# Kernel tuning notes

Hardware: AMD Instinct MI355X
Metric: run time of the kernel (lower is better)

Reference implementation:

```python
import jax, jax.numpy as jnp
import numpy as np

B, S, E = 2, 2048, 2048
H, D = 16, 128  # num_heads, head_dim = E // H


def setup_inputs() -> dict:
    key = jax.random.key(0)
    ks = jax.random.split(key, 5)
    hidden_states = jax.random.normal(ks[0], (B, S, E), dtype=jnp.float32) * 0.02
    wq = jax.random.normal(ks[1], (E, E), dtype=jnp.float32) * 0.02
    wk = jax.random.normal(ks[2], (E, E), dtype=jnp.float32) * 0.02
    wv = jax.random.normal(ks[3], (E, E), dtype=jnp.float32) * 0.02
    wo = jax.random.normal(ks[4], (E, E), dtype=jnp.float32) * 0.02
    bo = jnp.zeros((E,), dtype=jnp.float32)
    return {"hidden_states": hidden_states, "wq": wq, "wk": wk, "wv": wv, "wo": wo, "bo": bo}


def _split_heads(x):
    # [B, S, E] -> [B, H, S, D]
    return x.reshape(B, S, H, D).transpose(0, 2, 1, 3)


def reference(hidden_states, wq, wk, wv, wo, bo):
    q = _split_heads(hidden_states @ wq)  # [B,H,S,D]
    k = _split_heads(hidden_states @ wk)
    v = _split_heads(hidden_states @ wv)

    # GPT-Neo: no 1/sqrt(d) scaling; scores computed in fp32
    attn_weights = jnp.einsum("bhqd,bhkd->bhqk", q.astype(jnp.float32), k.astype(jnp.float32))

    causal_mask = jnp.tril(jnp.ones((S, S), dtype=bool))  # bias[:, :, :S, :S]
    # Faithful quirk: masked positions get the GLOBAL MIN of attn_weights, not -inf
    mask_value = jnp.min(attn_weights)
    attn_weights = jnp.where(causal_mask, attn_weights, mask_value)

    attn_weights = jax.nn.softmax(attn_weights, axis=-1).astype(v.dtype)
    attn_output = jnp.einsum("bhqk,bhkd->bhqd", attn_weights, v)  # [B,H,S,D]

    # merge heads: [B,H,S,D] -> [B,S,E]
    attn_output = attn_output.transpose(0, 2, 1, 3).reshape(B, S, E)
    attn_output = attn_output @ wo + bo
    return attn_output
```

## Files before the change

### kernel.cpp

```cpp
#include <hip/hip_runtime.h>

typedef unsigned short u16;
typedef unsigned int   u32;
typedef __attribute__((ext_vector_type(4))) float f32x4;
typedef __attribute__((ext_vector_type(4))) u32   u32x4;
typedef __attribute__((ext_vector_type(8))) __bf16 bf16x8;

#define S_LEN 2048
#define EMB   2048
#define NH    16
#define HD    128
#define NBH   32
#define MTOT  4096
#define NBMIN 512

__device__ __forceinline__ u16 f2bf(float f) {
    u32 u = __float_as_uint(f);
    return (u16)((u + 0x7FFFu + ((u >> 16) & 1u)) >> 16);
}
__device__ __forceinline__ float bf2f(u16 v) {
    return __uint_as_float(((u32)v) << 16);
}
__device__ __forceinline__ bf16x8 ld_frag(const u16* p) {
    return __builtin_bit_cast(bf16x8, *(const u32x4*)p);
}
__device__ __forceinline__ void gld_lds16(const void* g, void* l) {
    __builtin_amdgcn_global_load_lds(
        (__attribute__((address_space(1))) void*)(g),
        (__attribute__((address_space(3))) void*)(l), 16, 0, 0);
}

__global__ __launch_bounds__(256) void cast_x_kernel(
    const float* __restrict__ X, u16* __restrict__ Xb)
{
    const size_t i = ((size_t)blockIdx.x * 256 + threadIdx.x) * 8;
    float4 a = *(const float4*)&X[i];
    float4 b = *(const float4*)&X[i + 4];
    u32x4 o;
    o.x = (u32)f2bf(a.x) | ((u32)f2bf(a.y) << 16);
    o.y = (u32)f2bf(a.z) | ((u32)f2bf(a.w) << 16);
    o.z = (u32)f2bf(b.x) | ((u32)f2bf(b.y) << 16);
    o.w = (u32)f2bf(b.z) | ((u32)f2bf(b.w) << 16);
    *(u32x4*)&Xb[i] = o;
}

__global__ __launch_bounds__(256) void transpose_cast_w_kernel(
    const float* __restrict__ W0, const float* __restrict__ W1,
    const float* __restrict__ W2, const float* __restrict__ W3,
    u16* __restrict__ T0, u16* __restrict__ T1,
    u16* __restrict__ T2, u16* __restrict__ T3)
{
    __shared__ float Ls[64][68];
    const int t = threadIdx.x;
    const int n0 = blockIdx.x * 64, k0 = blockIdx.y * 64;
    const int z = blockIdx.z;
    const float* __restrict__ W = (z == 0) ? W0 : (z == 1) ? W1 : (z == 2) ? W2 : W3;
    u16* __restrict__ T = (z == 0) ? T0 : (z == 1) ? T1 : (z == 2) ? T2 : T3;

#pragma unroll
    for (int p = 0; p < 4; ++p) {
        const int r = (t >> 4) + 16 * p;
        const int c = (t & 15) * 4;
        *(float4*)&Ls[r][c] = *(const float4*)&W[(size_t)(k0 + r) * EMB + n0 + c];
    }
    __syncthreads();
    const int nl = t >> 2, q = t & 3;
    u32 pk[8];
#pragma unroll
    for (int j = 0; j < 8; ++j) {
        u16 lo = f2bf(Ls[q * 16 + 2 * j][nl]);
        u16 hi = f2bf(Ls[q * 16 + 2 * j + 1][nl]);
        pk[j] = (u32)lo | ((u32)hi << 16);
    }
    u32x4 o0 = {pk[0], pk[1], pk[2], pk[3]};
    u32x4 o1 = {pk[4], pk[5], pk[6], pk[7]};
    u16* dst = &T[(size_t)(n0 + nl) * EMB + k0 + q * 16];
    *(u32x4*)&dst[0] = o0;
    *(u32x4*)&dst[8] = o1;
}

__global__ __launch_bounds__(256) void transpose_v_kernel(
    const u16* __restrict__ V, u16* __restrict__ Vt)
{
    __shared__ u16 Ls[64][72];
    const int t = threadIdx.x;
    const int s0 = blockIdx.x * 64, d0 = blockIdx.y * 64, bh = blockIdx.z;
    const u16* __restrict__ src0 = V + ((size_t)bh * S_LEN) * HD;
    {
        const int r = t >> 2, c0 = (t & 3) * 16;
        const u16* src = &src0[(size_t)(s0 + r) * HD + d0 + c0];
        *(u32x4*)&Ls[r][c0]     = *(const u32x4*)&src[0];
        *(u32x4*)&Ls[r][c0 + 8] = *(const u32x4*)&src[8];
    }
    __syncthreads();
    const int dl = t >> 2, q = t & 3;
    u32 pk[8];
#pragma unroll
    for (int j = 0; j < 8; ++j) {
        u16 lo = Ls[q * 16 + 2 * j][dl];
        u16 hi = Ls[q * 16 + 2 * j + 1][dl];
        pk[j] = (u32)lo | ((u32)hi << 16);
    }
    u32x4 o0 = {pk[0], pk[1], pk[2], pk[3]};
    u32x4 o1 = {pk[4], pk[5], pk[6], pk[7]};
    u16* dst = &Vt[((size_t)bh * HD + d0 + dl) * S_LEN + s0 + q * 16];
    *(u32x4*)&dst[0] = o0;
    *(u32x4*)&dst[8] = o1;
}

__global__ __launch_bounds__(256) void gemm_qkv_mfma(
    const u16* __restrict__ Xb,
    const u16* __restrict__ Wtq, const u16* __restrict__ Wtk,
    const u16* __restrict__ Wtv,
    u16* __restrict__ Qo, u16* __restrict__ Ko, u16* __restrict__ Vo)
{
    __shared__ __attribute__((aligned(16))) u16 As[128 * 64];
    __shared__ __attribute__((aligned(16))) u16 Bs[128 * 64];
    const int t = threadIdx.x;
    const int w = t >> 6, lane = t & 63;
    const int wy = w >> 1, wx = w & 1;
    const int n0 = blockIdx.x * 128, m0 = blockIdx.y * 128;
    const int z = blockIdx.z;
    const u16* __restrict__ Wt = (z == 0) ? Wtq : (z == 1) ? Wtk : Wtv;
    u16* __restrict__ O = (z == 0) ? Qo : (z == 1) ? Ko : Vo;

    const int srow8 = lane >> 3;
    const int scol  = ((lane & 7) ^ srow8) * 8;
    const int fm = lane & 15, fk = (lane >> 4) * 8;
    const int key = (fm & 7) * 8;

    const u16* Ag = &Xb[(size_t)(m0 + w * 32 + srow8) * EMB + scol];
    const u16* Bg = &Wt[(size_t)(n0 + w * 32 + srow8) * EMB + scol];
    u16* const Al = &As[(w * 32) * 64];
    u16* const Bl = &Bs[(w * 32) * 64];

    f32x4 acc[4][4];
#pragma unroll
    for (int i = 0; i < 4; ++i)
#pragma unroll
        for (int j = 0; j < 4; ++j) acc[i][j] = (f32x4)0.0f;

    for (int k0 = 0; k0 < EMB; k0 += 64) {
        __syncthreads();
        gld_lds16(Ag + k0,               Al);
        gld_lds16(Ag + k0 + 8 * EMB,     Al + 8 * 64);
        gld_lds16(Ag + k0 + 16 * EMB,    Al + 16 * 64);
        gld_lds16(Ag + k0 + 24 * EMB,    Al + 24 * 64);
        gld_lds16(Bg + k0,               Bl);
        gld_lds16(Bg + k0 + 8 * EMB,     Bl + 8 * 64);
        gld_lds16(Bg + k0 + 16 * EMB,    Bl + 16 * 64);
        gld_lds16(Bg + k0 + 24 * EMB,    Bl + 24 * 64);
        __syncthreads();
#pragma unroll
        for (int dk2 = 0; dk2 < 2; ++dk2) {
            bf16x8 af[4], bfr[4];
#pragma unroll
            for (int mi = 0; mi < 4; ++mi)
                af[mi] = ld_frag(&As[(64 * wy + 16 * mi + fm) * 64
                                     + ((dk2 * 32 + fk) ^ key)]);
#pragma unroll
            for (int ni = 0; ni < 4; ++ni)
                bfr[ni] = ld_frag(&Bs[(64 * wx + 16 * ni + fm) * 64
                                      + ((dk2 * 32 + fk) ^ key)]);
#pragma unroll
            for (int mi = 0; mi < 4; ++mi)
#pragma unroll
                for (int ni = 0; ni < 4; ++ni)
                    acc[mi][ni] = __builtin_amdgcn_mfma_f32_16x16x32_bf16(
                        af[mi], bfr[ni], acc[mi][ni], 0, 0, 0);
        }
    }

    const int q4 = (lane >> 4) * 4;
#pragma unroll
    for (int mi = 0; mi < 4; ++mi)
#pragma unroll
        for (int ni = 0; ni < 4; ++ni) {
            const int n = n0 + 64 * wx + 16 * ni + (lane & 15);
            const int h = n >> 7, d = n & 127;
#pragma unroll
            for (int r = 0; r < 4; ++r) {
                const int m = m0 + 64 * wy + 16 * mi + q4 + r;
                const int bb = m >> 11, s = m & 2047;
                O[(((size_t)(bb * NH + h) * S_LEN) + s) * HD + d] = f2bf(acc[mi][ni][r]);
            }
        }
}

__global__ __launch_bounds__(256) void gemm_out_mfma(
    const u16* __restrict__ Ab, const u16* __restrict__ Wto,
    const float* __restrict__ bias, float* __restrict__ Out)
{
    __shared__ __attribute__((aligned(16))) u16 As[128 * 64];
    __shared__ __attribute__((aligned(16))) u16 Bs[64 * 64];
    const int t = threadIdx.x;
    const int w = t >> 6, lane = t & 63;
    const int wy = w >> 1, wx = w & 1;
    const int n0 = blockIdx.x * 64, m0 = blockIdx.y * 128;

    const int srow8 = lane >> 3;
    const int scol  = ((lane & 7) ^ srow8) * 8;
    const int fm = lane & 15, fk = (lane >> 4) * 8;
    const int key = (fm & 7) * 8;

    const u16* Ag = &Ab[(size_t)(m0 + w * 32 + srow8) * EMB + scol];
    const u16* Bg = &Wto[(size_t)(n0 + w * 16 + srow8) * EMB + scol];
    u16* const Al = &As[(w * 32) * 64];
    u16* const Bl = &Bs[(w * 16) * 64];

    f32x4 acc[4][2];
#pragma unroll
    for (int i = 0; i < 4; ++i)
#pragma unroll
        for (int j = 0; j < 2; ++j) acc[i][j] = (f32x4)0.0f;

    for (int k0 = 0; k0 < EMB; k0 += 64) {
        __syncthreads();
        gld_lds16(Ag + k0,               Al);
        gld_lds16(Ag + k0 + 8 * EMB,     Al + 8 * 64);
        gld_lds16(Ag + k0 + 16 * EMB,    Al + 16 * 64);
        gld_lds16(Ag + k0 + 24 * EMB,    Al + 24 * 64);
        gld_lds16(Bg + k0,               Bl);
        gld_lds16(Bg + k0 + 8 * EMB,     Bl + 8 * 64);
        __syncthreads();
#pragma unroll
        for (int dk2 = 0; dk2 < 2; ++dk2) {
            bf16x8 af[4], bfr[2];
#pragma unroll
            for (int mi = 0; mi < 4; ++mi)
                af[mi] = ld_frag(&As[(64 * wy + 16 * mi + fm) * 64
                                     + ((dk2 * 32 + fk) ^ key)]);
#pragma unroll
            for (int ni = 0; ni < 2; ++ni)
                bfr[ni] = ld_frag(&Bs[(32 * wx + 16 * ni + fm) * 64
                                      + ((dk2 * 32 + fk) ^ key)]);
#pragma unroll
            for (int mi = 0; mi < 4; ++mi)
#pragma unroll
                for (int ni = 0; ni < 2; ++ni)
                    acc[mi][ni] = __builtin_amdgcn_mfma_f32_16x16x32_bf16(
                        af[mi], bfr[ni], acc[mi][ni], 0, 0, 0);
        }
    }

    const int q4 = (lane >> 4) * 4;
#pragma unroll
    for (int mi = 0; mi < 4; ++mi)
#pragma unroll
        for (int ni = 0; ni < 2; ++ni) {
            const int n = n0 + 32 * wx + 16 * ni + (lane & 15);
            const float bv = bias[n];
#pragma unroll
            for (int r = 0; r < 4; ++r) {
                const int m = m0 + 64 * wy + 16 * mi + q4 + r;
                Out[(size_t)m * EMB + n] = acc[mi][ni][r] + bv;
            }
        }
}

__global__ __launch_bounds__(128) void vchunk_sum_kernel(
    const u16* __restrict__ V, float* __restrict__ csum)
{
    const int chunk = blockIdx.x, bh = blockIdx.y, d = threadIdx.x;
    const u16* vb = V + ((size_t)bh * S_LEN + chunk * 64) * HD + d;
    float s = 0.0f;
    for (int r = 0; r < 64; ++r) s += bf2f(vb[(size_t)r * HD]);
    csum[((size_t)bh * 32 + chunk) * HD + d] = s;
}

__global__ __launch_bounds__(128) void vsuffix_kernel(
    const u16* __restrict__ V, const float* __restrict__ csum,
    u16* __restrict__ vsuf)
{
    const int chunk = blockIdx.x, bh = blockIdx.y, d = threadIdx.x;
    float run = 0.0f;
    for (int c = 31; c > chunk; --c)
        run += csum[((size_t)bh * 32 + c) * HD + d];
    const size_t base = ((size_t)bh * S_LEN + chunk * 64) * HD + d;
    for (int r = 63; r >= 0; --r) {
        vsuf[base + (size_t)r * HD] = f2bf(run);
        run += bf2f(V[base + (size_t)r * HD]);
    }
}

__global__ __launch_bounds__(256) void attn_mfma(
    const u16* __restrict__ Q, const u16* __restrict__ K,
    const u16* __restrict__ Vt,
    u16* __restrict__ pacc0, u16* __restrict__ pacc1,
    float* __restrict__ den_p, float* __restrict__ blockmin)
{
    __shared__ __attribute__((aligned(16))) u16 Ps[128 * 136];
    __shared__ __attribute__((aligned(16))) u16 Cs[2][128 * 64];
    __shared__ float den_l[2][128];
    __shared__ float smn[256];

    const int t = threadIdx.x;
    const int w = t >> 6, lane = t & 63;
    const int wy = w >> 1, wx = w & 1;

    const int d_id = blockIdx.y * 16 + blockIdx.x;
    const int f_log = (d_id & 7) * 64 + (d_id >> 3);
    const int pp = (f_log & 15) >> 1, hpar = f_log & 1;
    const int bh = f_log >> 4;
    const int b = bh >> 4, h = bh & 15;

    const u16* __restrict__ Kg  = K + (size_t)bh * S_LEN * HD;
    const u16* __restrict__ Vtg = Vt + (size_t)bh * HD * S_LEN;
    u16* __restrict__ pacc = hpar ? pacc1 : pacc0;

    const int srow8 = lane >> 3;
    const int scol  = ((lane & 7) ^ srow8) * 8;
    const int fm = lane & 15, fk = (lane >> 4) * 8;
    const int key = (fm & 7) * 8;
    const int q4 = (lane >> 4) * 4;

#define STAGE_K(b_, j0_, h_) do { \
        const u16* g_ = &Kg[(size_t)((j0_) + w * 32 + srow8) * HD + (h_) * 64 + scol]; \
        u16* l_ = &Cs[b_][(w * 32) * 64]; \
        gld_lds16(g_,           l_); \
        gld_lds16(g_ + 8 * HD,  l_ + 8 * 64); \
        gld_lds16(g_ + 16 * HD, l_ + 16 * 64); \
        gld_lds16(g_ + 24 * HD, l_ + 24 * 64); } while (0)
#define STAGE_V(b_, j0_, h_) do { \
        const u16* g_ = &Vtg[(size_t)(w * 32 + srow8) * S_LEN + (j0_) + (h_) * 64 + scol]; \
        u16* l_ = &Cs[b_][(w * 32) * 64]; \
        gld_lds16(g_,              l_); \
        gld_lds16(g_ + 8 * S_LEN,  l_ + 8 * 64); \
        gld_lds16(g_ + 16 * S_LEN, l_ + 16 * 64); \
        gld_lds16(g_ + 24 * S_LEN, l_ + 24 * 64); } while (0)

    float mn = 3.0e38f;
    int c = 0;

    STAGE_K(0, hpar * 128, 0);
    __syncthreads();

    for (int pass = 0; pass < 2; ++pass) {
        const int qt = pass ? (15 - pp) : pp;
        const int i0 = qt * 128;
        const u16* __restrict__ Qg = Q + ((size_t)bh * S_LEN + i0) * HD;

        bf16x8 af[4][4];
#pragma unroll
        for (int mi = 0; mi < 4; ++mi)
#pragma unroll
            for (int dk = 0; dk < 4; ++dk)
                af[mi][dk] = ld_frag(
                    &Qg[(size_t)(64 * wy + 16 * mi + fm) * HD + dk * 32 + fk]);

        f32x4 oacc[4][4];
#pragma unroll
        for (int i = 0; i < 4; ++i)
#pragma unroll
            for (int j = 0; j < 4; ++j) oacc[i][j] = (f32x4)0.0f;
        float den[4][4] = {};

        for (int ji = 0; ji < 8; ++ji) {
            const int jt = hpar + 2 * ji;
            const int j0 = jt * 128;
            const bool causal = (jt <= qt);
            const bool hn = (ji < 7) || (pass == 0);
            const int nj0 = (ji < 7) ? (jt + 2) * 128 : hpar * 128;

            f32x4 sacc[4][4];
#pragma unroll
            for (int i = 0; i < 4; ++i)
#pragma unroll
                for (int j = 0; j < 4; ++j) sacc[i][j] = (f32x4)0.0f;

            STAGE_K(c ^ 1, j0, 1);
#pragma unroll
            for (int dk2 = 0; dk2 < 2; ++dk2) {
                bf16x8 bfr[4];
#pragma unroll
                for (int ni = 0; ni < 4; ++ni)
                    bfr[ni] = ld_frag(&Cs[c][(64 * wx + 16 * ni + fm) * 64
                                             + ((dk2 * 32 + fk) ^ key)]);
                __builtin_amdgcn_s_setprio(1);
#pragma unroll
                for (int mi = 0; mi < 4; ++mi)
#pragma unroll
                    for (int ni = 0; ni < 4; ++ni)
                        sacc[mi][ni] = __builtin_amdgcn_mfma_f32_16x16x32_bf16(
                            af[mi][dk2], bfr[ni], sacc[mi][ni], 0, 0, 0);
                __builtin_amdgcn_s_setprio(0);
            }
            __syncthreads();
            c ^= 1;

            if (causal)      STAGE_V(c ^ 1, j0, 0);
            else if (hn)     STAGE_K(c ^ 1, nj0, 0);
#pragma unroll
            for (int dk2 = 0; dk2 < 2; ++dk2) {
                bf16x8 bfr[4];
#pragma unroll
                for (int ni = 0; ni < 4; ++ni)
                    bfr[ni] = ld_frag(&Cs[c][(64 * wx + 16 * ni + fm) * 64
                                             + ((dk2 * 32 + fk) ^ key)]);
                __builtin_amdgcn_s_setprio(1);
#pragma unroll
                for (int mi = 0; mi < 4; ++mi)
#pragma unroll
                    for (int ni = 0; ni < 4; ++ni)
                        sacc[mi][ni] = __builtin_amdgcn_mfma_f32_16x16x32_bf16(
                            af[mi][2 + dk2], bfr[ni], sacc[mi][ni], 0, 0, 0);
                __builtin_amdgcn_s_setprio(0);
            }
            if (causal) {
                const bool dg = (jt == qt);
#pragma unroll
                for (int mi = 0; mi < 4; ++mi) {
                    const int rbase = 64 * wy + 16 * mi + q4;
#pragma unroll
                    for (int ni = 0; ni < 4; ++ni) {
                        const int cl = 64 * wx + 16 * ni + fm;
                        const int jg = j0 + cl;
#pragma unroll
                        for (int r = 0; r < 4; ++r) {
                            const float s = sacc[mi][ni][r];
                            mn = fminf(mn, s);
                            float e = __expf(s);
                            if (dg && jg > i0 + rbase + r) e = 0.0f;
                            den[mi][r] += e;
                            Ps[(rbase + r) * 136 + cl] = f2bf(e);
                        }
                    }
                }
            } else {
#pragma unroll
                for (int mi = 0; mi < 4; ++mi)
#pragma unroll
                    for (int ni = 0; ni < 4; ++ni)
#pragma unroll
                        for (int r = 0; r < 4; ++r)
                            mn = fminf(mn, sacc[mi][ni][r]);
            }
            __syncthreads();
            c ^= 1;

            if (causal) {
                STAGE_V(c ^ 1, j0, 1);
#pragma unroll
                for (int sk2 = 0; sk2 < 2; ++sk2) {
                    const int sk = sk2;
                    bf16x8 pa[4], pb[4];
#pragma unroll
                    for (int mi = 0; mi < 4; ++mi)
                        pa[mi] = ld_frag(&Ps[(64 * wy + 16 * mi + fm) * 136
                                             + sk * 32 + fk]);
#pragma unroll
                    for (int ni = 0; ni < 4; ++ni)
                        pb[ni] = ld_frag(&Cs[c][(64 * wx + 16 * ni + fm) * 64
                                                + ((sk2 * 32 + fk) ^ key)]);
                    __builtin_amdgcn_s_setprio(1);
#pragma unroll
                    for (int mi = 0; mi < 4; ++mi)
#pragma unroll
                        for (int ni = 0; ni < 4; ++ni)
                            oacc[mi][ni] = __builtin_amdgcn_mfma_f32_16x16x32_bf16(
                                pa[mi], pb[ni], oacc[mi][ni], 0, 0, 0);
                    __builtin_amdgcn_s_setprio(0);
                }
                __syncthreads();
                c ^= 1;

                if (hn) STAGE_K(c ^ 1, nj0, 0);
#pragma unroll
                for (int sk2 = 0; sk2 < 2; ++sk2) {
                    const int sk = 2 + sk2;
                    bf16x8 pa[4], pb[4];
#pragma unroll
                    for (int mi = 0; mi < 4; ++mi)
                        pa[mi] = ld_frag(&Ps[(64 * wy + 16 * mi + fm) * 136
                                             + sk * 32 + fk]);
#pragma unroll
                    for (int ni = 0; ni < 4; ++ni)
                        pb[ni] = ld_frag(&Cs[c][(64 * wx + 16 * ni + fm) * 64
                                                + ((sk2 * 32 + fk) ^ key)]);
                    __builtin_amdgcn_s_setprio(1);
#pragma unroll
                    for (int mi = 0; mi < 4; ++mi)
#pragma unroll
                        for (int ni = 0; ni < 4; ++ni)
                            oacc[mi][ni] = __builtin_amdgcn_mfma_f32_16x16x32_bf16(
                                pa[mi], pb[ni], oacc[mi][ni], 0, 0, 0);
                    __builtin_amdgcn_s_setprio(0);
                }
                __syncthreads();
                c ^= 1;
            }
        }

#pragma unroll
        for (int mi = 0; mi < 4; ++mi)
#pragma unroll
            for (int r = 0; r < 4; ++r) {
                float v = den[mi][r];
                v += __shfl_xor(v, 1, 64);
                v += __shfl_xor(v, 2, 64);
                v += __shfl_xor(v, 4, 64);
                v += __shfl_xor(v, 8, 64);
                den[mi][r] = v;
            }
        __syncthreads();
        if ((lane & 15) == 0) {
#pragma unroll
            for (int mi = 0; mi < 4; ++mi)
#pragma unroll
                for (int r = 0; r < 4; ++r)
                    den_l[wx][64 * wy + 16 * mi + q4 + r] = den[mi][r];
        }
        __syncthreads();
        if (t < 128)
            den_p[((size_t)hpar * NBH + bh) * S_LEN + i0 + t] =
                den_l[0][t] + den_l[1][t];

#pragma unroll
        for (int mi = 0; mi < 4; ++mi)
#pragma unroll
            for (int ni = 0; ni < 4; ++ni) {
                const int d = 64 * wx + 16 * ni + fm;
#pragma unroll
                for (int r = 0; r < 4; ++r) {
                    const int row = 64 * wy + 16 * mi + q4 + r;
                    pacc[((size_t)b * S_LEN + i0 + row) * EMB + h * HD + d] =
                        f2bf(oacc[mi][ni][r]);
                }
            }
        __syncthreads();
    }

    smn[t] = mn;
    __syncthreads();
    for (int sft = 128; sft > 0; sft >>= 1) {
        if (t < sft) smn[t] = fminf(smn[t], smn[t + sft]);
        __syncthreads();
    }
    if (t == 0) blockmin[d_id] = smn[0];

#undef STAGE_K
#undef STAGE_V
}

__global__ __launch_bounds__(256) void finalize_kernel(
    u16* __restrict__ outm, const u16* __restrict__ pacc1,
    const u16* __restrict__ vsuf, const float* __restrict__ den_p,
    const float* __restrict__ blockmin)
{
    __shared__ float wmin[4];
    const int t = threadIdx.x;
    float m = 3.0e38f;
    for (int ii = t; ii < NBMIN; ii += 256)
        m = fminf(m, blockmin[ii]);
    m = fminf(m, __shfl_xor(m, 1, 64));
    m = fminf(m, __shfl_xor(m, 2, 64));
    m = fminf(m, __shfl_xor(m, 4, 64));
    m = fminf(m, __shfl_xor(m, 8, 64));
    m = fminf(m, __shfl_xor(m, 16, 64));
    m = fminf(m, __shfl_xor(m, 32, 64));
    if ((t & 63) == 0) wmin[t >> 6] = m;
    __syncthreads();
    m = fminf(fminf(wmin[0], wmin[1]), fminf(wmin[2], wmin[3]));
    const float em = __expf(m);

    const size_t i = ((size_t)blockIdx.x * 256 + threadIdx.x) * 8;
    const int e = (int)(i & (EMB - 1));
    const int mm = (int)(i / EMB);
    const int b = mm >> 11, s = mm & 2047;
    const int hh = e >> 7, d = e & 127;
    const int bh = b * NH + hh;
    const float den = den_p[(size_t)bh * S_LEN + s]
                    + den_p[((size_t)NBH + bh) * S_LEN + s]
                    + (float)(S_LEN - 1 - s) * em;
    const float inv = 1.0f / den;
    u32x4 a = *(const u32x4*)&outm[i];
    u32x4 cc = *(const u32x4*)&pacc1[i];
    u32x4 vv = *(const u32x4*)&vsuf[((size_t)bh * S_LEN + s) * HD + d];
    const u16* pa = (const u16*)&a;
    const u16* pc = (const u16*)&cc;
    const u16* pv = (const u16*)&vv;
    u16 ov[8];
#pragma unroll
    for (int j = 0; j < 8; ++j) {
        const float v = bf2f(pa[j]) + bf2f(pc[j]) + em * bf2f(pv[j]);
        ov[j] = f2bf(v * inv);
    }
    *(u32x4*)&outm[i] = *(const u32x4*)ov;
}

extern "C" void kernel_launch(void* const* d_in, const int* in_sizes, int n_in,
                              void* d_out, int out_size, void* d_ws, size_t ws_size,
                              hipStream_t stream)
{
    (void)in_sizes; (void)n_in; (void)out_size; (void)ws_size;
    const float* hs = (const float*)d_in[0];
    const float* wq = (const float*)d_in[1];
    const float* wk = (const float*)d_in[2];
    const float* wv = (const float*)d_in[3];
    const float* wo = (const float*)d_in[4];
    const float* bo = (const float*)d_in[5];
    float* out = (float*)d_out;

    char* p = (char*)d_ws;
    const size_t TS = (size_t)NBH * S_LEN * HD;
    u16* Xb   = (u16*)p; p += (size_t)MTOT * EMB * 2;
    u16* Wtq  = (u16*)p; p += (size_t)EMB * EMB * 2;
    u16* Wtk  = (u16*)p; p += (size_t)EMB * EMB * 2;
    u16* Wtv  = (u16*)p; p += (size_t)EMB * EMB * 2;
    u16* Wto  = (u16*)p; p += (size_t)EMB * EMB * 2;
    u16* Qb   = (u16*)p; p += TS * 2;
    u16* Kb   = (u16*)p; p += TS * 2;
    u16* Vb   = (u16*)p; p += TS * 2;
    u16* Vtb  = (u16*)p; p += TS * 2;
    u16* outm = (u16*)p; p += (size_t)MTOT * EMB * 2;
    u16* vsuf = (u16*)p; p += TS * 2;
    float* csum     = (float*)p; p += (size_t)NBH * 32 * HD * 4;
    float* blockmin = (float*)p; p += 1024 * 4;
    float* den_p    = (float*)p; p += (size_t)2 * NBH * S_LEN * 4;
    u16* pacc1 = Xb;

    cast_x_kernel<<<4096, 256, 0, stream>>>(hs, Xb);
    transpose_cast_w_kernel<<<dim3(32, 32, 4), 256, 0, stream>>>(
        wq, wk, wv, wo, Wtq, Wtk, Wtv, Wto);

    gemm_qkv_mfma<<<dim3(EMB / 128, MTOT / 128, 3), 256, 0, stream>>>(
        Xb, Wtq, Wtk, Wtv, Qb, Kb, Vb);

    transpose_v_kernel<<<dim3(32, 2, NBH), 256, 0, stream>>>(Vb, Vtb);
    vchunk_sum_kernel<<<dim3(32, NBH), 128, 0, stream>>>(Vb, csum);
    vsuffix_kernel<<<dim3(32, NBH), 128, 0, stream>>>(Vb, csum, vsuf);

    attn_mfma<<<dim3(16, NBH), 256, 0, stream>>>(
        Qb, Kb, Vtb, outm, pacc1, den_p, blockmin);

    finalize_kernel<<<(MTOT * EMB / 8) / 256, 256, 0, stream>>>(
        outm, pacc1, vsuf, den_p, blockmin);

    gemm_out_mfma<<<dim3(EMB / 64, MTOT / 128), 256, 0, stream>>>(
        outm, Wto, bo, out);
}
```

Measured before the change: 441.2 us.

## Rewrite QKV GEMM as 256x256 double-buffered pipelined tile, widen out-proj tile

The QKV projection GEMM moves from 128x128 tiles with 4 waves to 256x256 tiles with 8 waves. It double-buffers the LDS stages, prefetching the next K-tile while MFMAs run, and splits each K step into four sub-phases separated by s_barrier with s_setprio raised around the MFMA bursts. The aim is to hide global-load latency and get more reuse per loaded byte. The output-projection GEMM is also widened from 64 to 128 columns per block, using the old QKV kernel body. The larger tiles raise register and LDS pressure (64KB of LDS per block), and the QKV grid shrinks to 384 blocks, which may underfill the GPU.

Measured after the change: 477.8 us. 8.3% more time.

```diff
diff --git a/kernel.cpp b/kernel.cpp
--- a/kernel.cpp
+++ b/kernel.cpp
@@ -108,11 +108,150 @@
     *(u32x4*)&dst[8] = o1;
 }
 
-__global__ __launch_bounds__(256) void gemm_qkv_mfma(
+__global__ __launch_bounds__(512, 2) void gemm_qkv_mfma(
     const u16* __restrict__ Xb,
     const u16* __restrict__ Wtq, const u16* __restrict__ Wtk,
     const u16* __restrict__ Wtv,
     u16* __restrict__ Qo, u16* __restrict__ Ko, u16* __restrict__ Vo)
+{
+    __shared__ __attribute__((aligned(16))) u16 As[2][256 * 64];
+    __shared__ __attribute__((aligned(16))) u16 Bs[2][256 * 64];
+    const int tid = threadIdx.x;
+    const int w = tid >> 6, lane = tid & 63;
+    const int wr = w >> 2, wc = w & 3;
+    const int n0 = blockIdx.x * 256, m0 = blockIdx.y * 256;
+    const int z = blockIdx.z;
+    const u16* __restrict__ Wt = (z == 0) ? Wtq : (z == 1) ? Wtk : Wtv;
+    u16* __restrict__ O = (z == 0) ? Qo : (z == 1) ? Ko : Vo;
+
+    const int w8 = w * 8, l8 = lane >> 3;
+    const int scol = ((lane & 7) ^ l8) * 8;
+    const int fm = lane & 15, fk = (lane >> 4) * 8;
+    const int key = (fm & 7) * 8;
+    const int q4 = (lane >> 4) * 4;
+
+    const u16* Ag = &Xb[(size_t)(m0 + w8 + l8) * EMB + scol];
+    const u16* Bg = &Wt[(size_t)(n0 + w8 + l8) * EMB + scol];
+
+#define SA(d_, t_, p_) gld_lds16(Ag + (size_t)((p_) * 64) * EMB + (t_) * 64, \
+                                 &As[d_][((p_) * 64 + w8) * 64])
+#define SB(d_, t_, p_) gld_lds16(Bg + (size_t)((p_) * 64) * EMB + (t_) * 64, \
+                                 &Bs[d_][((p_) * 64 + w8) * 64])
+
+    f32x4 acc[8][4];
+#pragma unroll
+    for (int i = 0; i < 8; ++i)
+#pragma unroll
+        for (int j = 0; j < 4; ++j) acc[i][j] = (f32x4)0.0f;
+
+    SA(0, 0, 0); SA(0, 0, 1); SA(0, 0, 2); SA(0, 0, 3);
+    SB(0, 0, 0); SB(0, 0, 1); SB(0, 0, 2); SB(0, 0, 3);
+    __syncthreads();
+
+    for (int t = 0; t < 32; ++t) {
+        const int s = t & 1, d = s ^ 1;
+        const u16* Asl = &As[s][0];
+        const u16* Bsl = &Bs[s][0];
+        bf16x8 af[4][2], bf[2][2][2];
+
+        if (t < 31) { SA(d, t + 1, 0); SA(d, t + 1, 1); SA(d, t + 1, 2); SA(d, t + 1, 3); }
+#pragma unroll
+        for (int mi = 0; mi < 4; ++mi)
+#pragma unroll
+            for (int ks = 0; ks < 2; ++ks)
+                af[mi][ks] = ld_frag(&Asl[(wr * 128 + mi * 16 + fm) * 64
+                                          + ((ks * 32 + fk) ^ key)]);
+#pragma unroll
+        for (int ni = 0; ni < 2; ++ni)
+#pragma unroll
+            for (int ks = 0; ks < 2; ++ks)
+                bf[0][ni][ks] = ld_frag(&Bsl[(wc * 64 + ni * 16 + fm) * 64
+                                             + ((ks * 32 + fk) ^ key)]);
+        __builtin_amdgcn_s_barrier();
+        __builtin_amdgcn_s_setprio(1);
+#pragma unroll
+        for (int mi = 0; mi < 4; ++mi)
+#pragma unroll
+            for (int ni = 0; ni < 2; ++ni)
+#pragma unroll
+                for (int ks = 0; ks < 2; ++ks)
+                    acc[mi][ni] = __builtin_amdgcn_mfma_f32_16x16x32_bf16(
+                        af[mi][ks], bf[0][ni][ks], acc[mi][ni], 0, 0, 0);
+        __builtin_amdgcn_s_setprio(0);
+
+        if (t < 31) { SB(d, t + 1, 0); SB(d, t + 1, 1); SB(d, t + 1, 2); SB(d, t + 1, 3); }
+#pragma unroll
+        for (int ni = 0; ni < 2; ++ni)
+#pragma unroll
+            for (int ks = 0; ks < 2; ++ks)
+                bf[1][ni][ks] = ld_frag(&Bsl[(wc * 64 + 32 + ni * 16 + fm) * 64
+                                             + ((ks * 32 + fk) ^ key)]);
+        __builtin_amdgcn_s_barrier();
+        __builtin_amdgcn_s_setprio(1);
+#pragma unroll
+        for (int mi = 0; mi < 4; ++mi)
+#pragma unroll
+            for (int ni = 0; ni < 2; ++ni)
+#pragma unroll
+                for (int ks = 0; ks < 2; ++ks)
+                    acc[mi][2 + ni] = __builtin_amdgcn_mfma_f32_16x16x32_bf16(
+                        af[mi][ks], bf[1][ni][ks], acc[mi][2 + ni], 0, 0, 0);
+        __builtin_amdgcn_s_setprio(0);
+
+#pragma unroll
+        for (int mi = 0; mi < 4; ++mi)
+#pragma unroll
+            for (int ks = 0; ks < 2; ++ks)
+                af[mi][ks] = ld_frag(&Asl[(wr * 128 + 64 + mi * 16 + fm) * 64
+                                          + ((ks * 32 + fk) ^ key)]);
+        __builtin_amdgcn_s_barrier();
+        __builtin_amdgcn_s_setprio(1);
+#pragma unroll
+        for (int mi = 0; mi < 4; ++mi)
+#pragma unroll
+            for (int ni = 0; ni < 2; ++ni)
+#pragma unroll
+                for (int ks = 0; ks < 2; ++ks)
+                    acc[4 + mi][2 + ni] = __builtin_amdgcn_mfma_f32_16x16x32_bf16(
+                        af[mi][ks], bf[1][ni][ks], acc[4 + mi][2 + ni], 0, 0, 0);
+        __builtin_amdgcn_s_setprio(0);
+
+        __builtin_amdgcn_s_barrier();
+        __builtin_amdgcn_s_setprio(1);
+#pragma unroll
+        for (int mi = 0; mi < 4; ++mi)
+#pragma unroll
+            for (int ni = 0; ni < 2; ++ni)
+#pragma unroll
+                for (int ks = 0; ks < 2; ++ks)
+                    acc[4 + mi][ni] = __builtin_amdgcn_mfma_f32_16x16x32_bf16(
+                        af[mi][ks], bf[0][ni][ks], acc[4 + mi][ni], 0, 0, 0);
+        __builtin_amdgcn_s_setprio(0);
+
+        __syncthreads();
+    }
+
+#pragma unroll
+    for (int mi8 = 0; mi8 < 8; ++mi8)
+#pragma unroll
+        for (int nj = 0; nj < 4; ++nj) {
+            const int n = n0 + wc * 64 + nj * 16 + fm;
+            const int h = n >> 7, dd = n & 127;
+#pragma unroll
+            for (int r = 0; r < 4; ++r) {
+                const int m = m0 + wr * 128 + mi8 * 16 + q4 + r;
+                const int bb = m >> 11, ss = m & 2047;
+                O[(((size_t)(bb * NH + h) * S_LEN) + ss) * HD + dd] =
+                    f2bf(acc[mi8][nj][r]);
+            }
+        }
+#undef SA
+#undef SB
+}
+
+__global__ __launch_bounds__(256) void gemm_out_mfma(
+    const u16* __restrict__ Ab, const u16* __restrict__ Wto,
+    const float* __restrict__ bias, float* __restrict__ Out)
 {
     __shared__ __attribute__((aligned(16))) u16 As[128 * 64];
     __shared__ __attribute__((aligned(16))) u16 Bs[128 * 64];
@@ -120,17 +259,14 @@
     const int w = t >> 6, lane = t & 63;
     const int wy = w >> 1, wx = w & 1;
     const int n0 = blockIdx.x * 128, m0 = blockIdx.y * 128;
-    const int z = blockIdx.z;
-    const u16* __restrict__ Wt = (z == 0) ? Wtq : (z == 1) ? Wtk : Wtv;
-    u16* __restrict__ O = (z == 0) ? Qo : (z == 1) ? Ko : Vo;
 
     const int srow8 = lane >> 3;
     const int scol  = ((lane & 7) ^ srow8) * 8;
     const int fm = lane & 15, fk = (lane >> 4) * 8;
     const int key = (fm & 7) * 8;
 
-    const u16* Ag = &Xb[(size_t)(m0 + w * 32 + srow8) * EMB + scol];
-    const u16* Bg = &Wt[(size_t)(n0 + w * 32 + srow8) * EMB + scol];
+    const u16* Ag = &Ab[(size_t)(m0 + w * 32 + srow8) * EMB + scol];
+    const u16* Bg = &Wto[(size_t)(n0 + w * 32 + srow8) * EMB + scol];
     u16* const Al = &As[(w * 32) * 64];
     u16* const Bl = &Bs[(w * 32) * 64];
 
@@ -177,78 +313,6 @@
 #pragma unroll
         for (int ni = 0; ni < 4; ++ni) {
             const int n = n0 + 64 * wx + 16 * ni + (lane & 15);
-            const int h = n >> 7, d = n & 127;
-#pragma unroll
-            for (int r = 0; r < 4; ++r) {
-                const int m = m0 + 64 * wy + 16 * mi + q4 + r;
-                const int bb = m >> 11, s = m & 2047;
-                O[(((size_t)(bb * NH + h) * S_LEN) + s) * HD + d] = f2bf(acc[mi][ni][r]);
-            }
-        }
-}
-
-__global__ __launch_bounds__(256) void gemm_out_mfma(
-    const u16* __restrict__ Ab, const u16* __restrict__ Wto,
-    const float* __restrict__ bias, float* __restrict__ Out)
-{
-    __shared__ __attribute__((aligned(16))) u16 As[128 * 64];
-    __shared__ __attribute__((aligned(16))) u16 Bs[64 * 64];
-    const int t = threadIdx.x;
-    const int w = t >> 6, lane = t & 63;
-    const int wy = w >> 1, wx = w & 1;
-    const int n0 = blockIdx.x * 64, m0 = blockIdx.y * 128;
-
-    const int srow8 = lane >> 3;
-    const int scol  = ((lane & 7) ^ srow8) * 8;
-    const int fm = lane & 15, fk = (lane >> 4) * 8;
-    const int key = (fm & 7) * 8;
-
-    const u16* Ag = &Ab[(size_t)(m0 + w * 32 + srow8) * EMB + scol];
-    const u16* Bg = &Wto[(size_t)(n0 + w * 16 + srow8) * EMB + scol];
-    u16* const Al = &As[(w * 32) * 64];
-    u16* const Bl = &Bs[(w * 16) * 64];
-
-    f32x4 acc[4][2];
-#pragma unroll
-    for (int i = 0; i < 4; ++i)
-#pragma unroll
-        for (int j = 0; j < 2; ++j) acc[i][j] = (f32x4)0.0f;
-
-    for (int k0 = 0; k0 < EMB; k0 += 64) {
-        __syncthreads();
-        gld_lds16(Ag + k0,               Al);
-        gld_lds16(Ag + k0 + 8 * EMB,     Al + 8 * 64);
-        gld_lds16(Ag + k0 + 16 * EMB,    Al + 16 * 64);
-        gld_lds16(Ag + k0 + 24 * EMB,    Al + 24 * 64);
-        gld_lds16(Bg + k0,               Bl);
-        gld_lds16(Bg + k0 + 8 * EMB,     Bl + 8 * 64);
-        __syncthreads();
-#pragma unroll
-        for (int dk2 = 0; dk2 < 2; ++dk2) {
-            bf16x8 af[4], bfr[2];
-#pragma unroll
-            for (int mi = 0; mi < 4; ++mi)
-                af[mi] = ld_frag(&As[(64 * wy + 16 * mi + fm) * 64
-                                     + ((dk2 * 32 + fk) ^ key)]);
-#pragma unroll
-            for (int ni = 0; ni < 2; ++ni)
-                bfr[ni] = ld_frag(&Bs[(32 * wx + 16 * ni + fm) * 64
-                                      + ((dk2 * 32 + fk) ^ key)]);
-#pragma unroll
-            for (int mi = 0; mi < 4; ++mi)
-#pragma unroll
-                for (int ni = 0; ni < 2; ++ni)
-                    acc[mi][ni] = __builtin_amdgcn_mfma_f32_16x16x32_bf16(
-                        af[mi], bfr[ni], acc[mi][ni], 0, 0, 0);
-        }
-    }
-
-    const int q4 = (lane >> 4) * 4;
-#pragma unroll
-    for (int mi = 0; mi < 4; ++mi)
-#pragma unroll
-        for (int ni = 0; ni < 2; ++ni) {
-            const int n = n0 + 32 * wx + 16 * ni + (lane & 15);
             const float bv = bias[n];
 #pragma unroll
             for (int r = 0; r < 4; ++r) {
@@ -623,7 +687,7 @@
     transpose_cast_w_kernel<<<dim3(32, 32, 4), 256, 0, stream>>>(
         wq, wk, wv, wo, Wtq, Wtk, Wtv, Wto);
 
-    gemm_qkv_mfma<<<dim3(EMB / 128, MTOT / 128, 3), 256, 0, stream>>>(
+    gemm_qkv_mfma<<<dim3(EMB / 256, MTOT / 256, 3), 512, 0, stream>>>(
         Xb, Wtq, Wtk, Wtv, Qb, Kb, Vb);
 
     transpose_v_kernel<<<dim3(32, 2, NBH), 256, 0, stream>>>(Vb, Vtb);
@@ -636,6 +700,6 @@
     finalize_kernel<<<(MTOT * EMB / 8) / 256, 256, 0, stream>>>(
         outm, pacc1, vsuf, den_p, blockmin);
 
-    gemm_out_mfma<<<dim3(EMB / 64, MTOT / 128), 256, 0, stream>>>(
+    gemm_out_mfma<<<dim3(EMB / 128, MTOT / 128), 256, 0, stream>>>(
         outm, Wto, bo, out);
 }
```
